# Optimization experiments

Hardware: AMD Instinct MI355X
Metric: run time of the kernel (lower is better)

The kernel has to match this reference:

```python
import jax, jax.numpy as jnp
import numpy as np

N = 100000
E = 3200000
H = 64

def _lin(k, fan_in, fan_out):
    k1, k2 = jax.random.split(k)
    lim = 1.0 / np.sqrt(fan_in)
    W = jax.random.uniform(k1, (fan_in, fan_out), minval=-lim, maxval=lim, dtype=jnp.float32)
    b = jax.random.uniform(k2, (fan_out,), minval=-lim, maxval=lim, dtype=jnp.float32)
    return W, b

def setup_inputs() -> dict:
    key = jax.random.key(0)
    ks = jax.random.split(key, 12)
    x = jax.random.normal(ks[0], (N, 6), dtype=jnp.float32)
    adj = jax.random.randint(ks[1], (2, E), 0, N, dtype=jnp.int64)
    W1, b1 = _lin(ks[2], 6, H)
    W2, b2 = _lin(ks[3], H, H)
    Wf1, bf1 = _lin(ks[4], H, H)
    Wf2, bf2 = _lin(ks[5], H, H)
    Ws1, bs1 = _lin(ks[6], H, 32)
    Ws2, bs2 = _lin(ks[7], 32, 1)
    Wt1, bt1 = _lin(ks[8], H, 32)
    Wt2, bt2 = _lin(ks[9], 32, 4)
    return dict(x=x, adj=adj, W1=W1, b1=b1, W2=W2, b2=b2, Wf1=Wf1, bf1=bf1,
                Wf2=Wf2, bf2=bf2, Ws1=Ws1, bs1=bs1, Ws2=Ws2, bs2=bs2,
                Wt1=Wt1, bt1=bt1, Wt2=Wt2, bt2=bt2)

def reference(x, adj, W1, b1, W2, b2, Wf1, bf1, Wf2, bf2,
              Ws1, bs1, Ws2, bs2, Wt1, bt1, Wt2, bt2):
    # cell encoder: Linear(6,H) -> ReLU -> Linear(H,H)
    h = jax.nn.relu(x @ W1 + b1) @ W2 + b2  # [N, H]
    # scatter-mean neighbor aggregation: neighbor_sum[i] = mean(h[adj[1][adj[0]==i]])
    src = adj[0]
    dst = adj[1]
    gathered = h[dst]  # [E, H]
    seg_sum = jax.ops.segment_sum(gathered, src, num_segments=N)  # [N, H]
    counts = jax.ops.segment_sum(jnp.ones((E,), dtype=h.dtype), src, num_segments=N)  # [N]
    neighbor_mean = seg_sum / jnp.maximum(counts, 1.0)[:, None]  # zero where no neighbors
    h = h + neighbor_mean
    h = jax.nn.relu(h @ Wf1 + bf1)
    h = jax.nn.relu(h @ Wf2 + bf2)
    error_scores = (jax.nn.relu(h @ Ws1 + bs1) @ Ws2 + bs2)[:, 0]  # [N]
    error_types = jax.nn.relu(h @ Wt1 + bt1) @ Wt2 + bt2  # [N, 4]
    return (error_scores, error_types)
```

## Files before the change

kernel.cpp:

```cpp
#include <hip/hip_runtime.h>
#include <hip/hip_fp16.h>

#define NN 100000
#define NE 3200000
#define H  64

#define BSHIFT 7
#define BNODES 128
#define NB ((NN + BNODES - 1) / BNODES)

#define PTHREADS 1024
#define PCHUNK   8192
#define PEPT     (PCHUNK / PTHREADS)
#define NPBLK    ((NE + PCHUNK - 1) / PCHUNK)

#define ECAP 5120

__global__ __launch_bounds__(256) void encoder_kernel(
    const float* __restrict__ x,
    const float* __restrict__ W1, const float* __restrict__ b1,
    const float* __restrict__ W2, const float* __restrict__ b2,
    const float* __restrict__ Wf1, const float* __restrict__ Wf2,
    const float* __restrict__ Ws1, const float* __restrict__ bs1,
    const float* __restrict__ Ws2, const float* __restrict__ bs2,
    const float* __restrict__ Wt1, const float* __restrict__ bt1,
    const float* __restrict__ Wt2, const float* __restrict__ bt2,
    int* __restrict__ bfill,
    float* __restrict__ wf1t, float* __restrict__ wf2t,
    float* __restrict__ wht,  float* __restrict__ bhead,
    float* __restrict__ wfin, float* __restrict__ bfin,
    __half* __restrict__ h16)
{
    __shared__ float sh1[4][H];
    const int tid  = threadIdx.x;
    const int slot = tid >> 6;
    const int f    = tid & 63;
    const int node = blockIdx.x * 4 + slot;

    if (blockIdx.x < 48) {
        const int e   = blockIdx.x * 256 + tid;
        const int a   = e >> 12;
        const int idx = e & 4095;
        const int k4  = idx >> 8;
        const int ff  = (idx >> 2) & 63;
        const int j   = idx & 3;
        if (a == 0)      wf1t[idx] = Wf1[k4 * 256 + j * 64 + ff];
        else if (a == 1) wf2t[idx] = Wf2[k4 * 256 + j * 64 + ff];
        else             wht[idx]  = (ff < 32) ? Ws1[k4 * 128 + j * 32 + ff]
                                               : Wt1[k4 * 128 + j * 32 + (ff - 32)];
    } else if (blockIdx.x == 48) {
        for (int i = tid; i < NB; i += 256) bfill[i] = 0;
        if (tid < 64) bhead[tid] = (tid < 32) ? bs1[tid] : bt1[tid - 32];
        if (tid < 160) {
            const int c = tid >> 5, jj = tid & 31;
            wfin[tid] = (c == 0) ? Ws2[jj] : Wt2[jj * 4 + (c - 1)];
        }
        if (tid < 5) bfin[tid] = (tid == 0) ? bs2[0] : bt2[tid - 1];
    }

    {
        float acc = b1[f];
        #pragma unroll
        for (int k = 0; k < 6; ++k)
            acc = fmaf(x[node * 6 + k], W1[k * H + f], acc);
        sh1[slot][f] = fmaxf(acc, 0.0f);
    }
    __syncthreads();
    {
        float acc = b2[f];
        #pragma unroll 8
        for (int k = 0; k < H; ++k)
            acc = fmaf(sh1[slot][k], W2[k * H + f], acc);
        h16[node * H + f] = __float2half(acc);
    }
}

__global__ __launch_bounds__(PTHREADS) void partition_kernel(
    const int* __restrict__ src, const int* __restrict__ dst,
    int* __restrict__ bfill, unsigned* __restrict__ staging)
{
    __shared__ unsigned stage[PCHUNK];
    __shared__ int gpos[PCHUNK];
    __shared__ int lh[NB];
    __shared__ int lcur[NB];
    __shared__ int gbase[NB];
    __shared__ int wtot[16];
    const int t = threadIdx.x;
    const int lane = t & 63;
    const int wid  = t >> 6;
    const int cbase = blockIdx.x * PCHUNK;
    const int cnt = min(PCHUNK, NE - cbase);

    for (int i = t; i < NB; i += PTHREADS) lh[i] = 0;
    __syncthreads();

    unsigned ent[PEPT];
    int bkt[PEPT];
    #pragma unroll
    for (int j = 0; j < PEPT; ++j) {
        const int idx = t + j * PTHREADS;
        if (idx < cnt) {
            const int s_ = src[cbase + idx];
            const int d_ = dst[cbase + idx];
            bkt[j] = s_ >> BSHIFT;
            ent[j] = (unsigned)d_ | ((unsigned)(s_ & (BNODES - 1)) << 17);
            atomicAdd(&lh[bkt[j]], 1);
        } else bkt[j] = -1;
    }
    __syncthreads();

    const int hv = (t < NB) ? lh[t] : 0;
    int incl = hv;
    #pragma unroll
    for (int off = 1; off < 64; off <<= 1) {
        const int n = __shfl_up(incl, off);
        if (lane >= off) incl += n;
    }
    if (lane == 63) wtot[wid] = incl;
    __syncthreads();
    if (wid == 0 && lane < 16) {
        const int v = wtot[lane];
        int s2 = v;
        #pragma unroll
        for (int off = 1; off < 16; off <<= 1) {
            const int n = __shfl_up(s2, off);
            if (lane >= off) s2 += n;
        }
        wtot[lane] = s2 - v;
    }
    __syncthreads();
    if (t < NB) {
        const int excl = incl - hv + wtot[wid];
        lh[t]   = excl;
        lcur[t] = excl;
        gbase[t] = t * ECAP + ((hv > 0) ? atomicAdd(&bfill[t], hv) : 0);
    }
    __syncthreads();

    #pragma unroll
    for (int j = 0; j < PEPT; ++j) {
        if (bkt[j] >= 0) {
            const int lp = atomicAdd(&lcur[bkt[j]], 1);
            stage[lp] = ent[j];
            gpos[lp]  = gbase[bkt[j]] + (lp - lh[bkt[j]]);
        }
    }
    __syncthreads();

    for (int i = t; i < cnt; i += PTHREADS)
        staging[gpos[i]] = stage[i];
}

__global__ __launch_bounds__(1024) void bucket_sort_kernel(
    const unsigned* __restrict__ staging, const int* __restrict__ bfill,
    int* __restrict__ sdst, int* __restrict__ offs, int* __restrict__ counts)
{
    __shared__ int ldst[ECAP];
    __shared__ int cntS[BNODES];
    __shared__ int scanS[BNODES];
    __shared__ int lstart[BNODES];
    __shared__ int lcur[BNODES];
    const int t = threadIdx.x;
    const int b = blockIdx.x;
    const int base0 = b * ECAP;
    const int ecnt  = bfill[b];

    if (t < BNODES) cntS[t] = 0;
    __syncthreads();
    for (int i = t; i < ecnt; i += 1024)
        atomicAdd(&cntS[staging[base0 + i] >> 17], 1);
    __syncthreads();
    if (t < BNODES) scanS[t] = (cntS[t] + 3) & ~3;
    __syncthreads();
    for (int off = 1; off < BNODES; off <<= 1) {
        int xv = 0;
        if (t >= off && t < BNODES) xv = scanS[t - off];
        __syncthreads();
        if (t >= off && t < BNODES) scanS[t] += xv;
        __syncthreads();
    }
    if (t < BNODES) {
        const int st = scanS[t] - ((cntS[t] + 3) & ~3);
        lstart[t] = st;
        lcur[t]   = st;
    }
    __syncthreads();
    const int tot4 = scanS[BNODES - 1];
    for (int i = t; i < ecnt; i += 1024) {
        const unsigned ev = staging[base0 + i];
        const int lp = atomicAdd(&lcur[(int)(ev >> 17)], 1);
        ldst[lp] = (int)(ev & 0x1FFFFu);
    }
    __syncthreads();
    for (int i = t; i < tot4; i += 1024)
        sdst[base0 + i] = ldst[i];

    const int nbase = b * BNODES;
    if (t < BNODES && nbase + t < NN) {
        offs[nbase + t]   = base0 + lstart[t];
        counts[nbase + t] = cntS[t];
    }
}

#define ACC4(cv, u)                                                            \
    {                                                                          \
        const float m = (rem > (u)) ? 1.0f : 0.0f;                             \
        const __half2* ph = reinterpret_cast<const __half2*>(&(cv));           \
        const float2 p0 = __half22float2(ph[0]);                               \
        const float2 p1 = __half22float2(ph[1]);                               \
        const float2 p2 = __half22float2(ph[2]);                               \
        const float2 p3 = __half22float2(ph[3]);                               \
        acc0 = fmaf(m, p0.x, acc0); acc1 = fmaf(m, p0.y, acc1);                \
        acc2 = fmaf(m, p1.x, acc2); acc3 = fmaf(m, p1.y, acc3);                \
        acc4 = fmaf(m, p2.x, acc4); acc5 = fmaf(m, p2.y, acc5);                \
        acc6 = fmaf(m, p3.x, acc6); acc7 = fmaf(m, p3.y, acc7);                \
    }

#define FLUSHN(jj)                                                             \
    {                                                                          \
        float4* w0 = reinterpret_cast<float4*>(&sp[r][g << 3]);                \
        w0[0] = make_float4(acc0, acc1, acc2, acc3);                           \
        w0[1] = make_float4(acc4, acc5, acc6, acc7);                           \
        const float ssum = sp[0][f] + sp[1][f] + sp[2][f] + sp[3][f]           \
                         + sp[4][f] + sp[5][f] + sp[6][f] + sp[7][f];          \
        const int dgj = DGf(jj);                                               \
        sa[jj][f] = SVf(jj) + ssum * (1.0f / fmaxf((float)dgj, 1.0f));         \
        acc0 = acc1 = acc2 = acc3 = acc4 = acc5 = acc6 = acc7 = 0.0f;          \
    }

#define GSTEP(c0, c1, c2, c3, n0_, n1_, n2_, n3_)                              \
    {                                                                          \
        if (jn < 4) {                       \
            const int rem = DGf(jn) - bn - 4 * r;                              \
            const int i0 = (rem > 0) ? idxN.x : 0;                             \
            const int i1 = (rem > 1) ? idxN.y : 0;                             \
            const int i2 = (rem > 2) ? idxN.z : 0;                             \
            const int i3 = (rem > 3) ? idxN.w : 0;                             \
            n0_ = *reinterpret_cast<const int4*>(hbase + ((size_t)i0 << 6));   \
            n1_ = *reinterpret_cast<const int4*>(hbase + ((size_t)i1 << 6));   \
            n2_ = *reinterpret_cast<const int4*>(hbase + ((size_t)i2 << 6));   \
            n3_ = *reinterpret_cast<const int4*>(hbase + ((size_t)i3 << 6));   \
        }                                                                      \
        int jm = jn, bm = bn; adv(jm, bm);                                     \
        idxN = IDXL(jm, bm);                                                   \
        {                                \
            const int rem = DGf(jc) - bc - 4 * r;                              \
            ACC4(c0, 0); ACC4(c1, 1); ACC4(c2, 2); ACC4(c3, 3);                \
        }                                                                      \
        if (jn != jc) FLUSHN(jc);                                              \
        jc = jn; bc = bn; jn = jm; bn = bm;                                    \
    }

__global__ __launch_bounds__(64, 4) void gather_head_kernel(
    const __half* __restrict__ h16,
    const int* __restrict__ counts, const int* __restrict__ offs,
    const int* __restrict__ sdst,
    const float* __restrict__ wf1t, const float* __restrict__ bf1,
    const float* __restrict__ wf2t, const float* __restrict__ bf2,
    const float* __restrict__ wht,  const float* __restrict__ bhead,
    const float* __restrict__ wfin, const float* __restrict__ bfin,
    float* __restrict__ out_scores, float* __restrict__ out_types)
{
    __shared__ float sa[4][H];
    __shared__ float sb[4][H];
    __shared__ float sp[8][H];
    const int f  = threadIdx.x;
    const int n0 = blockIdx.x * 4;
    const int g  = f & 7;
    const int r  = f >> 3;
    const __half* __restrict__ hbase = h16 + (g << 3);

    const int dg0 = counts[n0 + 0], dg1 = counts[n0 + 1],
              dg2 = counts[n0 + 2], dg3 = counts[n0 + 3];
    const int st0 = offs[n0 + 0], st1 = offs[n0 + 1],
              st2 = offs[n0 + 2], st3 = offs[n0 + 3];

    const float sv0 = __half2float(h16[((size_t)(n0 + 0) << 6) + f]);
    const float sv1 = __half2float(h16[((size_t)(n0 + 1) << 6) + f]);
    const float sv2 = __half2float(h16[((size_t)(n0 + 2) << 6) + f]);
    const float sv3 = __half2float(h16[((size_t)(n0 + 3) << 6) + f]);
    sa[0][f] = sv0; sa[1][f] = sv1; sa[2][f] = sv2; sa[3][f] = sv3;

    auto DGf = [&](int j) { return j == 0 ? dg0 : j == 1 ? dg1 : j == 2 ? dg2 : dg3; };
    auto STf = [&](int j) { return j == 0 ? st0 : j == 1 ? st1 : j == 2 ? st2 : st3; };
    auto SVf = [&](int j) { return j == 0 ? sv0 : j == 1 ? sv1 : j == 2 ? sv2 : sv3; };
    auto adv = [&](int& j, int& b) {
        if (j >= 4) return;
        b += 32;
        if (b >= DGf(j)) { b = 0; do { ++j; } while (j < 4 && DGf(j) == 0); }
    };
    auto IDXL = [&](int j, int b) -> int4 {
        if (j < 4) return *reinterpret_cast<const int4*>(&sdst[STf(j) + b + 4 * r]);
        return make_int4(0, 0, 0, 0);
    };

    float acc0 = 0.f, acc1 = 0.f, acc2 = 0.f, acc3 = 0.f,
          acc4 = 0.f, acc5 = 0.f, acc6 = 0.f, acc7 = 0.f;
    int4 A0 = make_int4(0,0,0,0), A1 = A0, A2 = A0, A3 = A0;
    int4 B0 = A0, B1 = A0, B2 = A0, B3 = A0;

    int jc = 0, bc = 0;
    while (jc < 4 && DGf(jc) == 0) ++jc;
    int jn = jc, bn = bc; adv(jn, bn);
    int4 idxC = IDXL(jc, bc);
    int4 idxN = IDXL(jn, bn);
    if (jc < 4) {
        const int rem = DGf(jc) - bc - 4 * r;
        const int i0 = (rem > 0) ? idxC.x : 0;
        const int i1 = (rem > 1) ? idxC.y : 0;
        const int i2 = (rem > 2) ? idxC.z : 0;
        const int i3 = (rem > 3) ? idxC.w : 0;
        A0 = *reinterpret_cast<const int4*>(hbase + ((size_t)i0 << 6));
        A1 = *reinterpret_cast<const int4*>(hbase + ((size_t)i1 << 6));
        A2 = *reinterpret_cast<const int4*>(hbase + ((size_t)i2 << 6));
        A3 = *reinterpret_cast<const int4*>(hbase + ((size_t)i3 << 6));
    }

    while (jc < 4) {
        GSTEP(A0, A1, A2, A3, B0, B1, B2, B3);
        if (jc >= 4) break;
        GSTEP(B0, B1, B2, B3, A0, A1, A2, A3);
    }

    {
        const float bb = bf1[f];
        float o0 = bb, o1 = bb, o2 = bb, o3 = bb;
        #pragma unroll
        for (int k4 = 0; k4 < 16; ++k4) {
            const float4 w  = *reinterpret_cast<const float4*>(&wf1t[(k4 * 64 + f) * 4]);
            const float4 a0 = *reinterpret_cast<const float4*>(&sa[0][k4 * 4]);
            const float4 a1 = *reinterpret_cast<const float4*>(&sa[1][k4 * 4]);
            const float4 a2 = *reinterpret_cast<const float4*>(&sa[2][k4 * 4]);
            const float4 a3 = *reinterpret_cast<const float4*>(&sa[3][k4 * 4]);
            o0 = fmaf(a0.x, w.x, o0); o0 = fmaf(a0.y, w.y, o0); o0 = fmaf(a0.z, w.z, o0); o0 = fmaf(a0.w, w.w, o0);
            o1 = fmaf(a1.x, w.x, o1); o1 = fmaf(a1.y, w.y, o1); o1 = fmaf(a1.z, w.z, o1); o1 = fmaf(a1.w, w.w, o1);
            o2 = fmaf(a2.x, w.x, o2); o2 = fmaf(a2.y, w.y, o2); o2 = fmaf(a2.z, w.z, o2); o2 = fmaf(a2.w, w.w, o2);
            o3 = fmaf(a3.x, w.x, o3); o3 = fmaf(a3.y, w.y, o3); o3 = fmaf(a3.z, w.z, o3); o3 = fmaf(a3.w, w.w, o3);
        }
        sb[0][f] = fmaxf(o0, 0.0f);
        sb[1][f] = fmaxf(o1, 0.0f);
        sb[2][f] = fmaxf(o2, 0.0f);
        sb[3][f] = fmaxf(o3, 0.0f);
    }

    {
        const float bb = bf2[f];
        float o0 = bb, o1 = bb, o2 = bb, o3 = bb;
        #pragma unroll
        for (int k4 = 0; k4 < 16; ++k4) {
            const float4 w  = *reinterpret_cast<const float4*>(&wf2t[(k4 * 64 + f) * 4]);
            const float4 a0 = *reinterpret_cast<const float4*>(&sb[0][k4 * 4]);
            const float4 a1 = *reinterpret_cast<const float4*>(&sb[1][k4 * 4]);
            const float4 a2 = *reinterpret_cast<const float4*>(&sb[2][k4 * 4]);
            const float4 a3 = *reinterpret_cast<const float4*>(&sb[3][k4 * 4]);
            o0 = fmaf(a0.x, w.x, o0); o0 = fmaf(a0.y, w.y, o0); o0 = fmaf(a0.z, w.z, o0); o0 = fmaf(a0.w, w.w, o0);
            o1 = fmaf(a1.x, w.x, o1); o1 = fmaf(a1.y, w.y, o1); o1 = fmaf(a1.z, w.z, o1); o1 = fmaf(a1.w, w.w, o1);
            o2 = fmaf(a2.x, w.x, o2); o2 = fmaf(a2.y, w.y, o2); o2 = fmaf(a2.z, w.z, o2); o2 = fmaf(a2.w, w.w, o2);
            o3 = fmaf(a3.x, w.x, o3); o3 = fmaf(a3.y, w.y, o3); o3 = fmaf(a3.z, w.z, o3); o3 = fmaf(a3.w, w.w, o3);
        }
        sa[0][f] = fmaxf(o0, 0.0f);
        sa[1][f] = fmaxf(o1, 0.0f);
        sa[2][f] = fmaxf(o2, 0.0f);
        sa[3][f] = fmaxf(o3, 0.0f);
    }

    {
        const float bb = bhead[f];
        float o0 = bb, o1 = bb, o2 = bb, o3 = bb;
        #pragma unroll
        for (int k4 = 0; k4 < 16; ++k4) {
            const float4 w  = *reinterpret_cast<const float4*>(&wht[(k4 * 64 + f) * 4]);
            const float4 a0 = *reinterpret_cast<const float4*>(&sa[0][k4 * 4]);
            const float4 a1 = *reinterpret_cast<const float4*>(&sa[1][k4 * 4]);
            const float4 a2 = *reinterpret_cast<const float4*>(&sa[2][k4 * 4]);
            const float4 a3 = *reinterpret_cast<const float4*>(&sa[3][k4 * 4]);
            o0 = fmaf(a0.x, w.x, o0); o0 = fmaf(a0.y, w.y, o0); o0 = fmaf(a0.z, w.z, o0); o0 = fmaf(a0.w, w.w, o0);
            o1 = fmaf(a1.x, w.x, o1); o1 = fmaf(a1.y, w.y, o1); o1 = fmaf(a1.z, w.z, o1); o1 = fmaf(a1.w, w.w, o1);
            o2 = fmaf(a2.x, w.x, o2); o2 = fmaf(a2.y, w.y, o2); o2 = fmaf(a2.z, w.z, o2); o2 = fmaf(a2.w, w.w, o2);
            o3 = fmaf(a3.x, w.x, o3); o3 = fmaf(a3.y, w.y, o3); o3 = fmaf(a3.z, w.z, o3); o3 = fmaf(a3.w, w.w, o3);
        }
        sb[0][f] = fmaxf(o0, 0.0f);
        sb[1][f] = fmaxf(o1, 0.0f);
        sb[2][f] = fmaxf(o2, 0.0f);
        sb[3][f] = fmaxf(o3, 0.0f);
    }

    {
        const int j = f >> 4;
        const int c = f & 15;
        if (c < 5) {
            float a2 = bfin[c];
            const int off = (c == 0) ? 0 : 32;
            const int rot = ((c << 2) + (j << 3)) & 31;
            #pragma unroll 8
            for (int jj = 0; jj < 32; ++jj) {
                const int q = (jj + rot) & 31;
                a2 = fmaf(sb[j][off + q], wfin[c * 32 + q], a2);
            }
            const int node = n0 + j;
            if (c == 0) out_scores[node] = a2;
            else        out_types[node * 4 + (c - 1)] = a2;
        }
    }
}

#undef GSTEP
#undef FLUSHN
#undef ACC4

extern "C" void kernel_launch(void* const* d_in, const int* in_sizes, int n_in,
                              void* d_out, int out_size, void* d_ws, size_t ws_size,
                              hipStream_t stream)
{
    const float* x   = (const float*)d_in[0];
    const int*   adj = (const int*)  d_in[1];
    const float* W1  = (const float*)d_in[2];
    const float* b1  = (const float*)d_in[3];
    const float* W2  = (const float*)d_in[4];
    const float* b2  = (const float*)d_in[5];
    const float* Wf1 = (const float*)d_in[6];
    const float* bf1 = (const float*)d_in[7];
    const float* Wf2 = (const float*)d_in[8];
    const float* bf2 = (const float*)d_in[9];
    const float* Ws1 = (const float*)d_in[10];
    const float* bs1 = (const float*)d_in[11];
    const float* Ws2 = (const float*)d_in[12];
    const float* bs2 = (const float*)d_in[13];
    const float* Wt1 = (const float*)d_in[14];
    const float* bt1 = (const float*)d_in[15];
    const float* Wt2 = (const float*)d_in[16];
    const float* bt2 = (const float*)d_in[17];

    float* out_scores = (float*)d_out;
    float* out_types  = out_scores + NN;

    unsigned* staging = (unsigned*)d_ws;
    int*      sdst    = (int*)(staging + (size_t)NB * ECAP);
    __half*   h16     = (__half*)(sdst + (size_t)NB * ECAP);
    int*      counts  = (int*)(h16 + (size_t)NN * H);
    int*      offs    = counts + NN;
    int*      bfill   = offs + NN;
    float*    wf1t    = (float*)(bfill + 784);
    float*    wf2t    = wf1t + 4096;
    float*    wht     = wf2t + 4096;
    float*    bhead   = wht + 4096;
    float*    wfin    = bhead + 64;
    float*    bfin    = wfin + 160;

    const int* src = adj;
    const int* dst = adj + NE;

    encoder_kernel<<<NN / 4, 256, 0, stream>>>(x, W1, b1, W2, b2,
                                               Wf1, Wf2, Ws1, bs1, Ws2, bs2,
                                               Wt1, bt1, Wt2, bt2,
                                               bfill, wf1t, wf2t, wht, bhead, wfin, bfin,
                                               h16);
    partition_kernel<<<NPBLK, PTHREADS, 0, stream>>>(src, dst, bfill, staging);
    bucket_sort_kernel<<<NB, 1024, 0, stream>>>(staging, bfill, sdst, offs, counts);
    gather_head_kernel<<<NN / 4, 64, 0, stream>>>(h16, counts, offs, sdst,
                                                  wf1t, bf1, wf2t, bf2,
                                                  wht, bhead, wfin, bfin,
                                                  out_scores, out_types);
}
```

Baseline: 278.7 us.

## Split weight prepack, batch encoder nodes per wave, vectorize partition and bucket sort

Moves weight transposition into a separate prepack kernel and adds a transposed W2 so the encoder computes four nodes per wave with float4 weight reads and shuffled x inputs. The partition kernel uses int4 loads of src/dst, and the bucket sort keeps its staged entries in registers instead of re-reading them, writing results with int4 stores. The gather/head kernel runs two independent waves per block. This targets global load efficiency and launch granularity, but adds an extra launch, and the bucket sort reads fixed 8192 slots per bucket beyond ECAP (masked out).

```diff
diff --git a/kernel.cpp b/kernel.cpp
--- a/kernel.cpp
+++ b/kernel.cpp
@@ -16,10 +16,8 @@
 
 #define ECAP 5120
 
-__global__ __launch_bounds__(256) void encoder_kernel(
-    const float* __restrict__ x,
-    const float* __restrict__ W1, const float* __restrict__ b1,
-    const float* __restrict__ W2, const float* __restrict__ b2,
+__global__ __launch_bounds__(256) void prepack_kernel(
+    const float* __restrict__ W2,
     const float* __restrict__ Wf1, const float* __restrict__ Wf2,
     const float* __restrict__ Ws1, const float* __restrict__ bs1,
     const float* __restrict__ Ws2, const float* __restrict__ bs2,
@@ -27,17 +25,11 @@
     const float* __restrict__ Wt2, const float* __restrict__ bt2,
     int* __restrict__ bfill,
     float* __restrict__ wf1t, float* __restrict__ wf2t,
-    float* __restrict__ wht,  float* __restrict__ bhead,
-    float* __restrict__ wfin, float* __restrict__ bfin,
-    __half* __restrict__ h16)
+    float* __restrict__ wht,  float* __restrict__ w2t,
+    float* __restrict__ bhead, float* __restrict__ wfin, float* __restrict__ bfin)
 {
-    __shared__ float sh1[4][H];
-    const int tid  = threadIdx.x;
-    const int slot = tid >> 6;
-    const int f    = tid & 63;
-    const int node = blockIdx.x * 4 + slot;
-
-    if (blockIdx.x < 48) {
+    const int tid = threadIdx.x;
+    if (blockIdx.x < 64) {
         const int e   = blockIdx.x * 256 + tid;
         const int a   = e >> 12;
         const int idx = e & 4095;
@@ -46,9 +38,10 @@
         const int j   = idx & 3;
         if (a == 0)      wf1t[idx] = Wf1[k4 * 256 + j * 64 + ff];
         else if (a == 1) wf2t[idx] = Wf2[k4 * 256 + j * 64 + ff];
-        else             wht[idx]  = (ff < 32) ? Ws1[k4 * 128 + j * 32 + ff]
+        else if (a == 2) wht[idx]  = (ff < 32) ? Ws1[k4 * 128 + j * 32 + ff]
                                                : Wt1[k4 * 128 + j * 32 + (ff - 32)];
-    } else if (blockIdx.x == 48) {
+        else             w2t[idx]  = W2[k4 * 256 + j * 64 + ff];
+    } else {
         for (int i = tid; i < NB; i += 256) bfill[i] = 0;
         if (tid < 64) bhead[tid] = (tid < 32) ? bs1[tid] : bt1[tid - 32];
         if (tid < 160) {
@@ -57,22 +50,53 @@
         }
         if (tid < 5) bfin[tid] = (tid == 0) ? bs2[0] : bt2[tid - 1];
     }
-
-    {
-        float acc = b1[f];
+}
+
+__global__ __launch_bounds__(256) void encoder_kernel(
+    const float* __restrict__ x,
+    const float* __restrict__ W1, const float* __restrict__ b1,
+    const float* __restrict__ w2t, const float* __restrict__ b2,
+    __half* __restrict__ h16)
+{
+    __shared__ float sh[16][H];
+    const int tid = threadIdx.x;
+    const int w   = tid >> 6;
+    const int f   = tid & 63;
+    const int nw  = blockIdx.x * 16 + w * 4;
+
+    const float xv = (f < 24) ? x[nw * 6 + f] : 0.0f;
+
+    const float bb1 = b1[f];
+    float w1r[6];
+    #pragma unroll
+    for (int k = 0; k < 6; ++k) w1r[k] = W1[k * H + f];
+
+    #pragma unroll
+    for (int j = 0; j < 4; ++j) {
+        float acc = bb1;
         #pragma unroll
         for (int k = 0; k < 6; ++k)
-            acc = fmaf(x[node * 6 + k], W1[k * H + f], acc);
-        sh1[slot][f] = fmaxf(acc, 0.0f);
-    }
-    __syncthreads();
-    {
-        float acc = b2[f];
-        #pragma unroll 8
-        for (int k = 0; k < H; ++k)
-            acc = fmaf(sh1[slot][k], W2[k * H + f], acc);
-        h16[node * H + f] = __float2half(acc);
-    }
+            acc = fmaf(__shfl(xv, j * 6 + k), w1r[k], acc);
+        sh[w * 4 + j][f] = fmaxf(acc, 0.0f);
+    }
+    const float bb2 = b2[f];
+    float o0 = bb2, o1 = bb2, o2 = bb2, o3 = bb2;
+    #pragma unroll
+    for (int k4 = 0; k4 < 16; ++k4) {
+        const float4 wv = *reinterpret_cast<const float4*>(&w2t[(k4 * 64 + f) * 4]);
+        const float4 a0 = *reinterpret_cast<const float4*>(&sh[w * 4 + 0][k4 * 4]);
+        const float4 a1 = *reinterpret_cast<const float4*>(&sh[w * 4 + 1][k4 * 4]);
+        const float4 a2 = *reinterpret_cast<const float4*>(&sh[w * 4 + 2][k4 * 4]);
+        const float4 a3 = *reinterpret_cast<const float4*>(&sh[w * 4 + 3][k4 * 4]);
+        o0 = fmaf(a0.x, wv.x, o0); o0 = fmaf(a0.y, wv.y, o0); o0 = fmaf(a0.z, wv.z, o0); o0 = fmaf(a0.w, wv.w, o0);
+        o1 = fmaf(a1.x, wv.x, o1); o1 = fmaf(a1.y, wv.y, o1); o1 = fmaf(a1.z, wv.z, o1); o1 = fmaf(a1.w, wv.w, o1);
+        o2 = fmaf(a2.x, wv.x, o2); o2 = fmaf(a2.y, wv.y, o2); o2 = fmaf(a2.z, wv.z, o2); o2 = fmaf(a2.w, wv.w, o2);
+        o3 = fmaf(a3.x, wv.x, o3); o3 = fmaf(a3.y, wv.y, o3); o3 = fmaf(a3.z, wv.z, o3); o3 = fmaf(a3.w, wv.w, o3);
+    }
+    h16[((size_t)(nw + 0) << 6) + f] = __float2half(o0);
+    h16[((size_t)(nw + 1) << 6) + f] = __float2half(o1);
+    h16[((size_t)(nw + 2) << 6) + f] = __float2half(o2);
+    h16[((size_t)(nw + 3) << 6) + f] = __float2half(o3);
 }
 
 __global__ __launch_bounds__(PTHREADS) void partition_kernel(
@@ -96,16 +120,32 @@
 
     unsigned ent[PEPT];
     int bkt[PEPT];
-    #pragma unroll
-    for (int j = 0; j < PEPT; ++j) {
-        const int idx = t + j * PTHREADS;
-        if (idx < cnt) {
-            const int s_ = src[cbase + idx];
-            const int d_ = dst[cbase + idx];
-            bkt[j] = s_ >> BSHIFT;
-            ent[j] = (unsigned)d_ | ((unsigned)(s_ & (BNODES - 1)) << 17);
+    const int tbase = t * PEPT;
+    if (tbase + PEPT <= cnt) {
+        const int4 s0 = *reinterpret_cast<const int4*>(&src[cbase + tbase]);
+        const int4 s1 = *reinterpret_cast<const int4*>(&src[cbase + tbase + 4]);
+        const int4 d0 = *reinterpret_cast<const int4*>(&dst[cbase + tbase]);
+        const int4 d1 = *reinterpret_cast<const int4*>(&dst[cbase + tbase + 4]);
+        const int sa_[8] = {s0.x, s0.y, s0.z, s0.w, s1.x, s1.y, s1.z, s1.w};
+        const int da_[8] = {d0.x, d0.y, d0.z, d0.w, d1.x, d1.y, d1.z, d1.w};
+        #pragma unroll
+        for (int j = 0; j < PEPT; ++j) {
+            bkt[j] = sa_[j] >> BSHIFT;
+            ent[j] = (unsigned)da_[j] | ((unsigned)(sa_[j] & (BNODES - 1)) << 17);
             atomicAdd(&lh[bkt[j]], 1);
-        } else bkt[j] = -1;
+        }
+    } else {
+        #pragma unroll
+        for (int j = 0; j < PEPT; ++j) {
+            const int idx = tbase + j;
+            if (idx < cnt) {
+                const int s_ = src[cbase + idx];
+                const int d_ = dst[cbase + idx];
+                bkt[j] = s_ >> BSHIFT;
+                ent[j] = (unsigned)d_ | ((unsigned)(s_ & (BNODES - 1)) << 17);
+                atomicAdd(&lh[bkt[j]], 1);
+            } else bkt[j] = -1;
+        }
     }
     __syncthreads();
 
@@ -167,9 +207,20 @@
 
     if (t < BNODES) cntS[t] = 0;
     __syncthreads();
-    for (int i = t; i < ecnt; i += 1024)
-        atomicAdd(&cntS[staging[base0 + i] >> 17], 1);
-    __syncthreads();
+
+    const uint4 e0 = *reinterpret_cast<const uint4*>(&staging[base0 + t * 4]);
+    const uint4 e1 = *reinterpret_cast<const uint4*>(&staging[base0 + 4096 + t * 4]);
+    const unsigned ev[8] = {e0.x, e0.y, e0.z, e0.w, e1.x, e1.y, e1.z, e1.w};
+    int iv[8];
+    #pragma unroll
+    for (int u = 0; u < 8; ++u)
+        iv[u] = (u < 4) ? (t * 4 + u) : (4096 + t * 4 + (u - 4));
+
+    #pragma unroll
+    for (int u = 0; u < 8; ++u)
+        if (iv[u] < ecnt) atomicAdd(&cntS[ev[u] >> 17], 1);
+    __syncthreads();
+
     if (t < BNODES) scanS[t] = (cntS[t] + 3) & ~3;
     __syncthreads();
     for (int off = 1; off < BNODES; off <<= 1) {
@@ -185,15 +236,19 @@
         lcur[t]   = st;
     }
     __syncthreads();
+
+    #pragma unroll
+    for (int u = 0; u < 8; ++u)
+        if (iv[u] < ecnt) {
+            const int lp = atomicAdd(&lcur[(int)(ev[u] >> 17)], 1);
+            ldst[lp] = (int)(ev[u] & 0x1FFFFu);
+        }
+    __syncthreads();
+
     const int tot4 = scanS[BNODES - 1];
-    for (int i = t; i < ecnt; i += 1024) {
-        const unsigned ev = staging[base0 + i];
-        const int lp = atomicAdd(&lcur[(int)(ev >> 17)], 1);
-        ldst[lp] = (int)(ev & 0x1FFFFu);
-    }
-    __syncthreads();
-    for (int i = t; i < tot4; i += 1024)
-        sdst[base0 + i] = ldst[i];
+    for (int i = t * 4; i < tot4; i += 4096)
+        *reinterpret_cast<int4*>(&sdst[base0 + i]) =
+            *reinterpret_cast<const int4*>(&ldst[i]);
 
     const int nbase = b * BNODES;
     if (t < BNODES && nbase + t < NN) {
@@ -218,13 +273,14 @@
 
 #define FLUSHN(jj)                                                             \
     {                                                                          \
-        float4* w0 = reinterpret_cast<float4*>(&sp[r][g << 3]);                \
+        float4* w0 = reinterpret_cast<float4*>(&sp[wv][r][g << 3]);            \
         w0[0] = make_float4(acc0, acc1, acc2, acc3);                           \
         w0[1] = make_float4(acc4, acc5, acc6, acc7);                           \
-        const float ssum = sp[0][f] + sp[1][f] + sp[2][f] + sp[3][f]           \
-                         + sp[4][f] + sp[5][f] + sp[6][f] + sp[7][f];          \
+        const float ssum = sp[wv][0][f] + sp[wv][1][f] + sp[wv][2][f]          \
+                         + sp[wv][3][f] + sp[wv][4][f] + sp[wv][5][f]          \
+                         + sp[wv][6][f] + sp[wv][7][f];                        \
         const int dgj = DGf(jj);                                               \
-        sa[jj][f] = SVf(jj) + ssum * (1.0f / fmaxf((float)dgj, 1.0f));         \
+        sa[lb + jj][f] = SVf(jj) + ssum * (1.0f / fmaxf((float)dgj, 1.0f));    \
         acc0 = acc1 = acc2 = acc3 = acc4 = acc5 = acc6 = acc7 = 0.0f;          \
     }
 
@@ -251,7 +307,7 @@
         jc = jn; bc = bn; jn = jm; bn = bm;                                    \
     }
 
-__global__ __launch_bounds__(64, 4) void gather_head_kernel(
+__global__ __launch_bounds__(128, 8) void gather_head_kernel(
     const __half* __restrict__ h16,
     const int* __restrict__ counts, const int* __restrict__ offs,
     const int* __restrict__ sdst,
@@ -261,11 +317,13 @@
     const float* __restrict__ wfin, const float* __restrict__ bfin,
     float* __restrict__ out_scores, float* __restrict__ out_types)
 {
-    __shared__ float sa[4][H];
-    __shared__ float sb[4][H];
-    __shared__ float sp[8][H];
-    const int f  = threadIdx.x;
-    const int n0 = blockIdx.x * 4;
+    __shared__ float sa[8][H];
+    __shared__ float sb[8][H];
+    __shared__ float sp[2][8][H];
+    const int f  = threadIdx.x & 63;
+    const int wv = threadIdx.x >> 6;
+    const int lb = wv * 4;
+    const int n0 = blockIdx.x * 8 + lb;
     const int g  = f & 7;
     const int r  = f >> 3;
     const __half* __restrict__ hbase = h16 + (g << 3);
@@ -279,7 +337,8 @@
     const float sv1 = __half2float(h16[((size_t)(n0 + 1) << 6) + f]);
     const float sv2 = __half2float(h16[((size_t)(n0 + 2) << 6) + f]);
     const float sv3 = __half2float(h16[((size_t)(n0 + 3) << 6) + f]);
-    sa[0][f] = sv0; sa[1][f] = sv1; sa[2][f] = sv2; sa[3][f] = sv3;
+    sa[lb + 0][f] = sv0; sa[lb + 1][f] = sv1;
+    sa[lb + 2][f] = sv2; sa[lb + 3][f] = sv3;
 
     auto DGf = [&](int j) { return j == 0 ? dg0 : j == 1 ? dg1 : j == 2 ? dg2 : dg3; };
     auto STf = [&](int j) { return j == 0 ? st0 : j == 1 ? st1 : j == 2 ? st2 : st3; };
@@ -328,19 +387,19 @@
         #pragma unroll
         for (int k4 = 0; k4 < 16; ++k4) {
             const float4 w  = *reinterpret_cast<const float4*>(&wf1t[(k4 * 64 + f) * 4]);
-            const float4 a0 = *reinterpret_cast<const float4*>(&sa[0][k4 * 4]);
-            const float4 a1 = *reinterpret_cast<const float4*>(&sa[1][k4 * 4]);
-            const float4 a2 = *reinterpret_cast<const float4*>(&sa[2][k4 * 4]);
-            const float4 a3 = *reinterpret_cast<const float4*>(&sa[3][k4 * 4]);
+            const float4 a0 = *reinterpret_cast<const float4*>(&sa[lb + 0][k4 * 4]);
+            const float4 a1 = *reinterpret_cast<const float4*>(&sa[lb + 1][k4 * 4]);
+            const float4 a2 = *reinterpret_cast<const float4*>(&sa[lb + 2][k4 * 4]);
+            const float4 a3 = *reinterpret_cast<const float4*>(&sa[lb + 3][k4 * 4]);
             o0 = fmaf(a0.x, w.x, o0); o0 = fmaf(a0.y, w.y, o0); o0 = fmaf(a0.z, w.z, o0); o0 = fmaf(a0.w, w.w, o0);
             o1 = fmaf(a1.x, w.x, o1); o1 = fmaf(a1.y, w.y, o1); o1 = fmaf(a1.z, w.z, o1); o1 = fmaf(a1.w, w.w, o1);
             o2 = fmaf(a2.x, w.x, o2); o2 = fmaf(a2.y, w.y, o2); o2 = fmaf(a2.z, w.z, o2); o2 = fmaf(a2.w, w.w, o2);
             o3 = fmaf(a3.x, w.x, o3); o3 = fmaf(a3.y, w.y, o3); o3 = fmaf(a3.z, w.z, o3); o3 = fmaf(a3.w, w.w, o3);
         }
-        sb[0][f] = fmaxf(o0, 0.0f);
-        sb[1][f] = fmaxf(o1, 0.0f);
-        sb[2][f] = fmaxf(o2, 0.0f);
-        sb[3][f] = fmaxf(o3, 0.0f);
+        sb[lb + 0][f] = fmaxf(o0, 0.0f);
+        sb[lb + 1][f] = fmaxf(o1, 0.0f);
+        sb[lb + 2][f] = fmaxf(o2, 0.0f);
+        sb[lb + 3][f] = fmaxf(o3, 0.0f);
     }
 
     {
@@ -349,19 +408,19 @@
         #pragma unroll
         for (int k4 = 0; k4 < 16; ++k4) {
             const float4 w  = *reinterpret_cast<const float4*>(&wf2t[(k4 * 64 + f) * 4]);
-            const float4 a0 = *reinterpret_cast<const float4*>(&sb[0][k4 * 4]);
-            const float4 a1 = *reinterpret_cast<const float4*>(&sb[1][k4 * 4]);
-            const float4 a2 = *reinterpret_cast<const float4*>(&sb[2][k4 * 4]);
-            const float4 a3 = *reinterpret_cast<const float4*>(&sb[3][k4 * 4]);
+            const float4 a0 = *reinterpret_cast<const float4*>(&sb[lb + 0][k4 * 4]);
+            const float4 a1 = *reinterpret_cast<const float4*>(&sb[lb + 1][k4 * 4]);
+            const float4 a2 = *reinterpret_cast<const float4*>(&sb[lb + 2][k4 * 4]);
+            const float4 a3 = *reinterpret_cast<const float4*>(&sb[lb + 3][k4 * 4]);
             o0 = fmaf(a0.x, w.x, o0); o0 = fmaf(a0.y, w.y, o0); o0 = fmaf(a0.z, w.z, o0); o0 = fmaf(a0.w, w.w, o0);
             o1 = fmaf(a1.x, w.x, o1); o1 = fmaf(a1.y, w.y, o1); o1 = fmaf(a1.z, w.z, o1); o1 = fmaf(a1.w, w.w, o1);
             o2 = fmaf(a2.x, w.x, o2); o2 = fmaf(a2.y, w.y, o2); o2 = fmaf(a2.z, w.z, o2); o2 = fmaf(a2.w, w.w, o2);
             o3 = fmaf(a3.x, w.x, o3); o3 = fmaf(a3.y, w.y, o3); o3 = fmaf(a3.z, w.z, o3); o3 = fmaf(a3.w, w.w, o3);
         }
-        sa[0][f] = fmaxf(o0, 0.0f);
-        sa[1][f] = fmaxf(o1, 0.0f);
-        sa[2][f] = fmaxf(o2, 0.0f);
-        sa[3][f] = fmaxf(o3, 0.0f);
+        sa[lb + 0][f] = fmaxf(o0, 0.0f);
+        sa[lb + 1][f] = fmaxf(o1, 0.0f);
+        sa[lb + 2][f] = fmaxf(o2, 0.0f);
+        sa[lb + 3][f] = fmaxf(o3, 0.0f);
     }
 
     {
@@ -370,19 +429,19 @@
         #pragma unroll
         for (int k4 = 0; k4 < 16; ++k4) {
             const float4 w  = *reinterpret_cast<const float4*>(&wht[(k4 * 64 + f) * 4]);
-            const float4 a0 = *reinterpret_cast<const float4*>(&sa[0][k4 * 4]);
-            const float4 a1 = *reinterpret_cast<const float4*>(&sa[1][k4 * 4]);
-            const float4 a2 = *reinterpret_cast<const float4*>(&sa[2][k4 * 4]);
-            const float4 a3 = *reinterpret_cast<const float4*>(&sa[3][k4 * 4]);
+            const float4 a0 = *reinterpret_cast<const float4*>(&sa[lb + 0][k4 * 4]);
+            const float4 a1 = *reinterpret_cast<const float4*>(&sa[lb + 1][k4 * 4]);
+            const float4 a2 = *reinterpret_cast<const float4*>(&sa[lb + 2][k4 * 4]);
+            const float4 a3 = *reinterpret_cast<const float4*>(&sa[lb + 3][k4 * 4]);
             o0 = fmaf(a0.x, w.x, o0); o0 = fmaf(a0.y, w.y, o0); o0 = fmaf(a0.z, w.z, o0); o0 = fmaf(a0.w, w.w, o0);
             o1 = fmaf(a1.x, w.x, o1); o1 = fmaf(a1.y, w.y, o1); o1 = fmaf(a1.z, w.z, o1); o1 = fmaf(a1.w, w.w, o1);
             o2 = fmaf(a2.x, w.x, o2); o2 = fmaf(a2.y, w.y, o2); o2 = fmaf(a2.z, w.z, o2); o2 = fmaf(a2.w, w.w, o2);
             o3 = fmaf(a3.x, w.x, o3); o3 = fmaf(a3.y, w.y, o3); o3 = fmaf(a3.z, w.z, o3); o3 = fmaf(a3.w, w.w, o3);
         }
-        sb[0][f] = fmaxf(o0, 0.0f);
-        sb[1][f] = fmaxf(o1, 0.0f);
-        sb[2][f] = fmaxf(o2, 0.0f);
-        sb[3][f] = fmaxf(o3, 0.0f);
+        sb[lb + 0][f] = fmaxf(o0, 0.0f);
+        sb[lb + 1][f] = fmaxf(o1, 0.0f);
+        sb[lb + 2][f] = fmaxf(o2, 0.0f);
+        sb[lb + 3][f] = fmaxf(o3, 0.0f);
     }
 
     {
@@ -395,7 +454,7 @@
             #pragma unroll 8
             for (int jj = 0; jj < 32; ++jj) {
                 const int q = (jj + rot) & 31;
-                a2 = fmaf(sb[j][off + q], wfin[c * 32 + q], a2);
+                a2 = fmaf(sb[lb + j][off + q], wfin[c * 32 + q], a2);
             }
             const int node = n0 + j;
             if (c == 0) out_scores[node] = a2;
@@ -443,22 +502,23 @@
     float*    wf1t    = (float*)(bfill + 784);
     float*    wf2t    = wf1t + 4096;
     float*    wht     = wf2t + 4096;
-    float*    bhead   = wht + 4096;
+    float*    w2t     = wht + 4096;
+    float*    bhead   = w2t + 4096;
     float*    wfin    = bhead + 64;
     float*    bfin    = wfin + 160;
 
     const int* src = adj;
     const int* dst = adj + NE;
 
-    encoder_kernel<<<NN / 4, 256, 0, stream>>>(x, W1, b1, W2, b2,
-                                               Wf1, Wf2, Ws1, bs1, Ws2, bs2,
-                                               Wt1, bt1, Wt2, bt2,
-                                               bfill, wf1t, wf2t, wht, bhead, wfin, bfin,
-                                               h16);
+    prepack_kernel<<<65, 256, 0, stream>>>(W2, Wf1, Wf2, Ws1, bs1, Ws2, bs2,
+                                           Wt1, bt1, Wt2, bt2,
+                                           bfill, wf1t, wf2t, wht, w2t,
+                                           bhead, wfin, bfin);
+    encoder_kernel<<<NN / 16, 256, 0, stream>>>(x, W1, b1, w2t, b2, h16);
     partition_kernel<<<NPBLK, PTHREADS, 0, stream>>>(src, dst, bfill, staging);
     bucket_sort_kernel<<<NB, 1024, 0, stream>>>(staging, bfill, sdst, offs, counts);
-    gather_head_kernel<<<NN / 4, 64, 0, stream>>>(h16, counts, offs, sdst,
-                                                  wf1t, bf1, wf2t, bf2,
-                                                  wht, bhead, wfin, bfin,
-                                                  out_scores, out_types);
+    gather_head_kernel<<<NN / 8, 128, 0, stream>>>(h16, counts, offs, sdst,
+                                                   wf1t, bf1, wf2t, bf2,
+                                                   wht, bhead, wfin, bfin,
+                                                   out_scores, out_types);
 }
```

After: 417.5 us. +49.8%, slower.

## Fuse encoder, edge partition and weight prep into one heterogeneous kernel

Applied to the files above, without the earlier changes.

The encoder, partition and weight-transpose kernels become one launch whose block ranges do different jobs, and the bucket-fill reset moves to a memset. The encoder now handles 4 nodes per wave and keeps W2 in LDS, reading it as float4. The partition path loads edges with int4 vector loads, and bucket sort holds its entries in registers and writes with int4 stores. This removes a launch boundary and lets encoder work overlap partitioning, but the 1024-thread blocks with 75KB of LDS apply to the encoder blocks too, which may limit occupancy.

```diff
diff --git a/kernel.cpp b/kernel.cpp
--- a/kernel.cpp
+++ b/kernel.cpp
@@ -16,139 +16,197 @@
 
 #define ECAP 5120
 
-__global__ __launch_bounds__(256) void encoder_kernel(
+#define NENC ((NN + 63) / 64)
+#define NPRE 65
+#define NFUSED (NPBLK + NENC + NPRE)
+
+__global__ __launch_bounds__(1024, 8) void fused_pre_kernel(
+    const int* __restrict__ src, const int* __restrict__ dst,
+    int* __restrict__ bfill, unsigned* __restrict__ staging,
     const float* __restrict__ x,
     const float* __restrict__ W1, const float* __restrict__ b1,
     const float* __restrict__ W2, const float* __restrict__ b2,
+    __half* __restrict__ h16,
     const float* __restrict__ Wf1, const float* __restrict__ Wf2,
     const float* __restrict__ Ws1, const float* __restrict__ bs1,
     const float* __restrict__ Ws2, const float* __restrict__ bs2,
     const float* __restrict__ Wt1, const float* __restrict__ bt1,
     const float* __restrict__ Wt2, const float* __restrict__ bt2,
-    int* __restrict__ bfill,
     float* __restrict__ wf1t, float* __restrict__ wf2t,
     float* __restrict__ wht,  float* __restrict__ bhead,
-    float* __restrict__ wfin, float* __restrict__ bfin,
-    __half* __restrict__ h16)
+    float* __restrict__ wfin, float* __restrict__ bfin)
 {
-    __shared__ float sh1[4][H];
-    const int tid  = threadIdx.x;
-    const int slot = tid >> 6;
-    const int f    = tid & 63;
-    const int node = blockIdx.x * 4 + slot;
-
-    if (blockIdx.x < 48) {
-        const int e   = blockIdx.x * 256 + tid;
-        const int a   = e >> 12;
-        const int idx = e & 4095;
-        const int k4  = idx >> 8;
-        const int ff  = (idx >> 2) & 63;
-        const int j   = idx & 3;
-        if (a == 0)      wf1t[idx] = Wf1[k4 * 256 + j * 64 + ff];
-        else if (a == 1) wf2t[idx] = Wf2[k4 * 256 + j * 64 + ff];
-        else             wht[idx]  = (ff < 32) ? Ws1[k4 * 128 + j * 32 + ff]
-                                               : Wt1[k4 * 128 + j * 32 + (ff - 32)];
-    } else if (blockIdx.x == 48) {
-        for (int i = tid; i < NB; i += 256) bfill[i] = 0;
-        if (tid < 64) bhead[tid] = (tid < 32) ? bs1[tid] : bt1[tid - 32];
-        if (tid < 160) {
-            const int c = tid >> 5, jj = tid & 31;
-            wfin[tid] = (c == 0) ? Ws2[jj] : Wt2[jj * 4 + (c - 1)];
-        }
-        if (tid < 5) bfin[tid] = (tid == 0) ? bs2[0] : bt2[tid - 1];
-    }
-
-    {
-        float acc = b1[f];
+    __shared__ __align__(16) char smem[75008];
+    const int t   = threadIdx.x;
+    const int blk = blockIdx.x;
+
+    if (blk < NPBLK) {
+        unsigned* stage = (unsigned*)smem;
+        int*      gpos  = (int*)(smem + 32768);
+        int*      lh    = (int*)(smem + 65536);
+        int*      lcur  = (int*)(smem + 65536 + 3136);
+        int*      gbase = (int*)(smem + 65536 + 6272);
+        int*      wtot  = (int*)(smem + 65536 + 9408);
+
+        const int lane = t & 63;
+        const int wid  = t >> 6;
+        const int cbase = blk * PCHUNK;
+        const int cnt = min(PCHUNK, NE - cbase);
+
+        for (int i = t; i < NB; i += PTHREADS) lh[i] = 0;
+        __syncthreads();
+
+        unsigned ent[PEPT];
+        int bkt[PEPT];
+        const int tbase = t * PEPT;
+        if (tbase + PEPT <= cnt) {
+            const int4 s0 = *reinterpret_cast<const int4*>(&src[cbase + tbase]);
+            const int4 s1 = *reinterpret_cast<const int4*>(&src[cbase + tbase + 4]);
+            const int4 d0 = *reinterpret_cast<const int4*>(&dst[cbase + tbase]);
+            const int4 d1 = *reinterpret_cast<const int4*>(&dst[cbase + tbase + 4]);
+            const int sa_[8] = {s0.x, s0.y, s0.z, s0.w, s1.x, s1.y, s1.z, s1.w};
+            const int da_[8] = {d0.x, d0.y, d0.z, d0.w, d1.x, d1.y, d1.z, d1.w};
+            #pragma unroll
+            for (int j = 0; j < PEPT; ++j) {
+                bkt[j] = sa_[j] >> BSHIFT;
+                ent[j] = (unsigned)da_[j] | ((unsigned)(sa_[j] & (BNODES - 1)) << 17);
+                atomicAdd(&lh[bkt[j]], 1);
+            }
+        } else {
+            #pragma unroll
+            for (int j = 0; j < PEPT; ++j) {
+                const int idx = tbase + j;
+                if (idx < cnt) {
+                    const int s_ = src[cbase + idx];
+                    const int d_ = dst[cbase + idx];
+                    bkt[j] = s_ >> BSHIFT;
+                    ent[j] = (unsigned)d_ | ((unsigned)(s_ & (BNODES - 1)) << 17);
+                    atomicAdd(&lh[bkt[j]], 1);
+                } else bkt[j] = -1;
+            }
+        }
+        __syncthreads();
+
+        const int hv = (t < NB) ? lh[t] : 0;
+        int incl = hv;
         #pragma unroll
-        for (int k = 0; k < 6; ++k)
-            acc = fmaf(x[node * 6 + k], W1[k * H + f], acc);
-        sh1[slot][f] = fmaxf(acc, 0.0f);
-    }
-    __syncthreads();
-    {
-        float acc = b2[f];
-        #pragma unroll 8
-        for (int k = 0; k < H; ++k)
-            acc = fmaf(sh1[slot][k], W2[k * H + f], acc);
-        h16[node * H + f] = __float2half(acc);
-    }
-}
-
-__global__ __launch_bounds__(PTHREADS) void partition_kernel(
-    const int* __restrict__ src, const int* __restrict__ dst,
-    int* __restrict__ bfill, unsigned* __restrict__ staging)
-{
-    __shared__ unsigned stage[PCHUNK];
-    __shared__ int gpos[PCHUNK];
-    __shared__ int lh[NB];
-    __shared__ int lcur[NB];
-    __shared__ int gbase[NB];
-    __shared__ int wtot[16];
-    const int t = threadIdx.x;
-    const int lane = t & 63;
-    const int wid  = t >> 6;
-    const int cbase = blockIdx.x * PCHUNK;
-    const int cnt = min(PCHUNK, NE - cbase);
-
-    for (int i = t; i < NB; i += PTHREADS) lh[i] = 0;
-    __syncthreads();
-
-    unsigned ent[PEPT];
-    int bkt[PEPT];
-    #pragma unroll
-    for (int j = 0; j < PEPT; ++j) {
-        const int idx = t + j * PTHREADS;
-        if (idx < cnt) {
-            const int s_ = src[cbase + idx];
-            const int d_ = dst[cbase + idx];
-            bkt[j] = s_ >> BSHIFT;
-            ent[j] = (unsigned)d_ | ((unsigned)(s_ & (BNODES - 1)) << 17);
-            atomicAdd(&lh[bkt[j]], 1);
-        } else bkt[j] = -1;
-    }
-    __syncthreads();
-
-    const int hv = (t < NB) ? lh[t] : 0;
-    int incl = hv;
-    #pragma unroll
-    for (int off = 1; off < 64; off <<= 1) {
-        const int n = __shfl_up(incl, off);
-        if (lane >= off) incl += n;
-    }
-    if (lane == 63) wtot[wid] = incl;
-    __syncthreads();
-    if (wid == 0 && lane < 16) {
-        const int v = wtot[lane];
-        int s2 = v;
+        for (int off = 1; off < 64; off <<= 1) {
+            const int n = __shfl_up(incl, off);
+            if (lane >= off) incl += n;
+        }
+        if (lane == 63) wtot[wid] = incl;
+        __syncthreads();
+        if (wid == 0 && lane < 16) {
+            const int v = wtot[lane];
+            int s2 = v;
+            #pragma unroll
+            for (int off = 1; off < 16; off <<= 1) {
+                const int n = __shfl_up(s2, off);
+                if (lane >= off) s2 += n;
+            }
+            wtot[lane] = s2 - v;
+        }
+        __syncthreads();
+        if (t < NB) {
+            const int excl = incl - hv + wtot[wid];
+            lh[t]   = excl;
+            lcur[t] = excl;
+            gbase[t] = t * ECAP + ((hv > 0) ? atomicAdd(&bfill[t], hv) : 0);
+        }
+        __syncthreads();
+
         #pragma unroll
-        for (int off = 1; off < 16; off <<= 1) {
-            const int n = __shfl_up(s2, off);
-            if (lane >= off) s2 += n;
-        }
-        wtot[lane] = s2 - v;
-    }
-    __syncthreads();
-    if (t < NB) {
-        const int excl = incl - hv + wtot[wid];
-        lh[t]   = excl;
-        lcur[t] = excl;
-        gbase[t] = t * ECAP + ((hv > 0) ? atomicAdd(&bfill[t], hv) : 0);
-    }
-    __syncthreads();
-
-    #pragma unroll
-    for (int j = 0; j < PEPT; ++j) {
-        if (bkt[j] >= 0) {
-            const int lp = atomicAdd(&lcur[bkt[j]], 1);
-            stage[lp] = ent[j];
-            gpos[lp]  = gbase[bkt[j]] + (lp - lh[bkt[j]]);
-        }
-    }
-    __syncthreads();
-
-    for (int i = t; i < cnt; i += PTHREADS)
-        staging[gpos[i]] = stage[i];
+        for (int j = 0; j < PEPT; ++j) {
+            if (bkt[j] >= 0) {
+                const int lp = atomicAdd(&lcur[bkt[j]], 1);
+                stage[lp] = ent[j];
+                gpos[lp]  = gbase[bkt[j]] + (lp - lh[bkt[j]]);
+            }
+        }
+        __syncthreads();
+
+        for (int i = t; i < cnt; i += PTHREADS)
+            staging[gpos[i]] = stage[i];
+
+    } else if (blk < NPBLK + NENC) {
+        float* sh  = (float*)smem;
+        float* w2s = (float*)(smem + 16384);
+
+        {
+            const int i4 = t * 4;
+            const float4 wv4 = *reinterpret_cast<const float4*>(&W2[i4]);
+            const int k = i4 >> 6, f0 = i4 & 63;
+            const int dbase = (k >> 2) * 256 + (k & 3);
+            w2s[dbase + (f0 + 0) * 4] = wv4.x;
+            w2s[dbase + (f0 + 1) * 4] = wv4.y;
+            w2s[dbase + (f0 + 2) * 4] = wv4.z;
+            w2s[dbase + (f0 + 3) * 4] = wv4.w;
+        }
+        __syncthreads();
+
+        const int w  = t >> 6;
+        const int f  = t & 63;
+        const int nw = (blk - NPBLK) * 64 + w * 4;
+        if (nw < NN) {
+            const float xv = (f < 24) ? x[nw * 6 + f] : 0.0f;
+
+            const float bb1 = b1[f];
+            float w1r[6];
+            #pragma unroll
+            for (int k = 0; k < 6; ++k) w1r[k] = W1[k * H + f];
+
+            #pragma unroll
+            for (int j = 0; j < 4; ++j) {
+                float acc = bb1;
+                #pragma unroll
+                for (int k = 0; k < 6; ++k)
+                    acc = fmaf(__shfl(xv, j * 6 + k), w1r[k], acc);
+                sh[(w * 4 + j) * H + f] = fmaxf(acc, 0.0f);
+            }
+            const float bb2 = b2[f];
+            float o0 = bb2, o1 = bb2, o2 = bb2, o3 = bb2;
+            #pragma unroll
+            for (int k4 = 0; k4 < 16; ++k4) {
+                const float4 wv = *reinterpret_cast<const float4*>(&w2s[(k4 * 64 + f) * 4]);
+                const float4 a0 = *reinterpret_cast<const float4*>(&sh[(w * 4 + 0) * H + k4 * 4]);
+                const float4 a1 = *reinterpret_cast<const float4*>(&sh[(w * 4 + 1) * H + k4 * 4]);
+                const float4 a2 = *reinterpret_cast<const float4*>(&sh[(w * 4 + 2) * H + k4 * 4]);
+                const float4 a3 = *reinterpret_cast<const float4*>(&sh[(w * 4 + 3) * H + k4 * 4]);
+                o0 = fmaf(a0.x, wv.x, o0); o0 = fmaf(a0.y, wv.y, o0); o0 = fmaf(a0.z, wv.z, o0); o0 = fmaf(a0.w, wv.w, o0);
+                o1 = fmaf(a1.x, wv.x, o1); o1 = fmaf(a1.y, wv.y, o1); o1 = fmaf(a1.z, wv.z, o1); o1 = fmaf(a1.w, wv.w, o1);
+                o2 = fmaf(a2.x, wv.x, o2); o2 = fmaf(a2.y, wv.y, o2); o2 = fmaf(a2.z, wv.z, o2); o2 = fmaf(a2.w, wv.w, o2);
+                o3 = fmaf(a3.x, wv.x, o3); o3 = fmaf(a3.y, wv.y, o3); o3 = fmaf(a3.z, wv.z, o3); o3 = fmaf(a3.w, wv.w, o3);
+            }
+            h16[((size_t)(nw + 0) << 6) + f] = __float2half(o0);
+            h16[((size_t)(nw + 1) << 6) + f] = __float2half(o1);
+            h16[((size_t)(nw + 2) << 6) + f] = __float2half(o2);
+            h16[((size_t)(nw + 3) << 6) + f] = __float2half(o3);
+        }
+
+    } else {
+        const int pb = blk - NPBLK - NENC;
+        if (pb < 64) {
+            if (t < 256) {
+                const int e   = pb * 256 + t;
+                const int a   = e >> 12;
+                const int idx = e & 4095;
+                const int k4  = idx >> 8;
+                const int ff  = (idx >> 2) & 63;
+                const int j   = idx & 3;
+                if (a == 0)      wf1t[idx] = Wf1[k4 * 256 + j * 64 + ff];
+                else if (a == 1) wf2t[idx] = Wf2[k4 * 256 + j * 64 + ff];
+                else if (a == 2) wht[idx]  = (ff < 32) ? Ws1[k4 * 128 + j * 32 + ff]
+                                                       : Wt1[k4 * 128 + j * 32 + (ff - 32)];
+            }
+        } else {
+            if (t < 64) bhead[t] = (t < 32) ? bs1[t] : bt1[t - 32];
+            if (t < 160) {
+                const int c = t >> 5, jj = t & 31;
+                wfin[t] = (c == 0) ? Ws2[jj] : Wt2[jj * 4 + (c - 1)];
+            }
+            if (t < 5) bfin[t] = (t == 0) ? bs2[0] : bt2[t - 1];
+        }
+    }
 }
 
 __global__ __launch_bounds__(1024) void bucket_sort_kernel(
@@ -167,9 +225,22 @@
 
     if (t < BNODES) cntS[t] = 0;
     __syncthreads();
-    for (int i = t; i < ecnt; i += 1024)
-        atomicAdd(&cntS[staging[base0 + i] >> 17], 1);
+
+    const uint4 e0 = *reinterpret_cast<const uint4*>(&staging[base0 + t * 4]);
+    uint4 e1 = make_uint4(0u, 0u, 0u, 0u);
+    if (ecnt > 4096)
+        e1 = *reinterpret_cast<const uint4*>(&staging[base0 + 4096 + t * 4]);
+    const unsigned ev[8] = {e0.x, e0.y, e0.z, e0.w, e1.x, e1.y, e1.z, e1.w};
+    int iv[8];
+    #pragma unroll
+    for (int u = 0; u < 8; ++u)
+        iv[u] = (u < 4) ? (t * 4 + u) : (4096 + t * 4 + (u - 4));
+
+    #pragma unroll
+    for (int u = 0; u < 8; ++u)
+        if (iv[u] < ecnt) atomicAdd(&cntS[ev[u] >> 17], 1);
     __syncthreads();
+
     if (t < BNODES) scanS[t] = (cntS[t] + 3) & ~3;
     __syncthreads();
     for (int off = 1; off < BNODES; off <<= 1) {
@@ -185,15 +256,19 @@
         lcur[t]   = st;
     }
     __syncthreads();
+
+    #pragma unroll
+    for (int u = 0; u < 8; ++u)
+        if (iv[u] < ecnt) {
+            const int lp = atomicAdd(&lcur[(int)(ev[u] >> 17)], 1);
+            ldst[lp] = (int)(ev[u] & 0x1FFFFu);
+        }
+    __syncthreads();
+
     const int tot4 = scanS[BNODES - 1];
-    for (int i = t; i < ecnt; i += 1024) {
-        const unsigned ev = staging[base0 + i];
-        const int lp = atomicAdd(&lcur[(int)(ev >> 17)], 1);
-        ldst[lp] = (int)(ev & 0x1FFFFu);
-    }
-    __syncthreads();
-    for (int i = t; i < tot4; i += 1024)
-        sdst[base0 + i] = ldst[i];
+    for (int i = t * 4; i < tot4; i += 4096)
+        *reinterpret_cast<int4*>(&sdst[base0 + i]) =
+            *reinterpret_cast<const int4*>(&ldst[i]);
 
     const int nbase = b * BNODES;
     if (t < BNODES && nbase + t < NN) {
@@ -450,12 +525,12 @@
     const int* src = adj;
     const int* dst = adj + NE;
 
-    encoder_kernel<<<NN / 4, 256, 0, stream>>>(x, W1, b1, W2, b2,
-                                               Wf1, Wf2, Ws1, bs1, Ws2, bs2,
-                                               Wt1, bt1, Wt2, bt2,
-                                               bfill, wf1t, wf2t, wht, bhead, wfin, bfin,
-                                               h16);
-    partition_kernel<<<NPBLK, PTHREADS, 0, stream>>>(src, dst, bfill, staging);
+    hipMemsetAsync(bfill, 0, NB * sizeof(int), stream);
+    fused_pre_kernel<<<NFUSED, PTHREADS, 0, stream>>>(
+        src, dst, bfill, staging,
+        x, W1, b1, W2, b2, h16,
+        Wf1, Wf2, Ws1, bs1, Ws2, bs2, Wt1, bt1, Wt2, bt2,
+        wf1t, wf2t, wht, bhead, wfin, bfin);
     bucket_sort_kernel<<<NB, 1024, 0, stream>>>(staging, bfill, sdst, offs, counts);
     gather_head_kernel<<<NN / 4, 64, 0, stream>>>(h16, counts, offs, sdst,
                                                   wf1t, bf1, wf2t, bf2,
```

Result: faster. 242.6 us (median of 2 runs) (-13.0%).
